# Kernel optimization log

Measured on AMD Instinct MI355X. Metric: run time of the kernel, lower is better.

Reference implementation:

```python
import jax, jax.numpy as jnp
import numpy as np

# Dims (from module defaults / forward default)
I, H, L, P = 99, 256, 2, 9   # input_size, hidden_size, num_layers, num_predictions*len(quantiles)
B, T, DEC = 64, 128, 325     # batch, encoder seq len, decoder steps (max_timesteps)


def setup_inputs() -> dict:
    key = jax.random.key(0)
    ks = jax.random.split(key, 16)
    k = 1.0 / np.sqrt(H)
    u = lambda kk, shape: jax.random.uniform(kk, shape, jnp.float32, -k, k)
    return {
        "x": jax.random.normal(ks[0], (B, T, I), jnp.float32),
        # LSTM layer 0 (input -> hidden), torch gate order i,f,g,o; b = b_ih + b_hh fused
        "W_ih0": u(ks[1], (4 * H, I)), "W_hh0": u(ks[2], (4 * H, H)), "b0": u(ks[3], (4 * H,)),
        # LSTM layer 1 (hidden -> hidden)
        "W_ih1": u(ks[4], (4 * H, H)), "W_hh1": u(ks[5], (4 * H, H)), "b1": u(ks[6], (4 * H,)),
        # linear head: ReLU -> Linear(H, I)
        "W_lin": u(ks[7], (I, H)), "b_lin": u(ks[8], (I,)),
        # prediction head: ReLU -> Linear(H, H//2) -> ReLU -> Linear(H//2, P)  (dropout = eval identity)
        "W_p1": u(ks[9], (H // 2, H)), "b_p1": u(ks[10], (H // 2,)),
        "W_p2": u(ks[11], (P, H // 2)), "b_p2": u(ks[12], (P,)),
    }


def _cell(xt, h, c, W_ih, W_hh, b):
    # single LSTM step; xt:[B,Din] h,c:[B,H]
    gates = xt @ W_ih.T + h @ W_hh.T + b
    i, f, g, o = jnp.split(gates, 4, axis=-1)
    c = jax.nn.sigmoid(f) * c + jax.nn.sigmoid(i) * jnp.tanh(g)
    h = jax.nn.sigmoid(o) * jnp.tanh(c)
    return h, c


def _lstm_seq(x, W_ih, W_hh, b, h0, c0):
    # x:[B,T,Din] -> outputs [B,T,H], final (h,c)
    xW = jnp.einsum('btd,gd->btg', x, W_ih) + b  # precompute input projection

    def step(carry, xw_t):
        h, c = carry
        gates = xw_t + h @ W_hh.T
        i, f, g, o = jnp.split(gates, 4, axis=-1)
        c = jax.nn.sigmoid(f) * c + jax.nn.sigmoid(i) * jnp.tanh(g)
        h = jax.nn.sigmoid(o) * jnp.tanh(c)
        return (h, c), h

    (h, c), hs = jax.lax.scan(step, (h0, c0), jnp.swapaxes(xW, 0, 1))
    return jnp.swapaxes(hs, 0, 1), h, c


def _lin_head(h, W, b):
    return jnp.maximum(h, 0.0) @ W.T + b


def _pred_head(h, W1, b1, W2, b2):
    z = jnp.maximum(jnp.maximum(h, 0.0) @ W1.T + b1, 0.0)
    return z @ W2.T + b2


def reference(x, W_ih0, W_hh0, b0, W_ih1, W_hh1, b1,
              W_lin, b_lin, W_p1, b_p1, W_p2, b_p2):
    Bx = x.shape[0]
    z = jnp.zeros((Bx, H), x.dtype)
    # encoder: 2-layer LSTM, zero initial state
    out0, h0_, c0_ = _lstm_seq(x, W_ih0, W_hh0, b0, z, z)
    out1, h1_, c1_ = _lstm_seq(out0, W_ih1, W_hh1, b1, z, z)

    yields_back = _pred_head(out1, W_p1, b_p1, W_p2, b_p2)        # [B,T,P]
    sensors_back = _lin_head(out1, W_lin, b_lin)                  # [B,T,I]
    dec_in = jax.lax.stop_gradient(sensors_back[:, -1, :])        # [B,I]

    def dec_step(carry, _):
        h0, c0, h1, c1, xin = carry
        h0, c0 = _cell(xin, h0, c0, W_ih0, W_hh0, b0)
        h1, c1 = _cell(h0, h1, c1, W_ih1, W_hh1, b1)
        sens = _lin_head(h1, W_lin, b_lin)                        # [B,I]
        yld = _pred_head(h1, W_p1, b_p1, W_p2, b_p2)              # [B,P]
        xin = jax.lax.stop_gradient(sens)
        return (h0, c0, h1, c1, xin), (sens, yld)

    _, (sens_fwd, yld_fwd) = jax.lax.scan(
        dec_step, (h0_, c0_, h1_, c1_, dec_in), None, length=DEC)
    sensors_forward = jnp.swapaxes(sens_fwd, 0, 1)                # [B,DEC,I]
    yields = jnp.concatenate([yields_back, jnp.swapaxes(yld_fwd, 0, 1)], axis=1)  # [B,T+DEC,P]
    return (sensors_forward, sensors_back, yields)
```

## Files before the change

kernel.cpp:

```cpp
#include <hip/hip_runtime.h>
#include <math.h>


#define NW    128
#define NTHR  256

#define II 99
#define BB 64
#define TT 128
#define DD 325
#define QTOT 453
#define PPQ 9

#define SF_OFF 0
#define SB_OFF (BB*DD*II)
#define Y_OFF  (SB_OFF + BB*TT*II)

#define WS_H0 1024
#define WS_H1 (WS_H0 + 2*256*64)
#define WS_Z  (WS_H1 + 2*256*64)
#define WS_XT (WS_Z  + 2*128*64)

#define AGENT __HIP_MEMORY_SCOPE_AGENT

__device__ __forceinline__ float sigm(float v){ return 1.0f/(1.0f+expf(-v)); }
__device__ __forceinline__ void st_wt(float* p, float v){ __hip_atomic_store(p, v, __ATOMIC_RELAXED, AGENT); }

__device__ __forceinline__ void fma32(float acc[32], float4 w0, float4 w1, float4 hv) {
  float wr[8] = {w0.x,w0.y,w0.z,w0.w,w1.x,w1.y,w1.z,w1.w};
  #pragma unroll
  for (int g = 0; g < 8; ++g) {
    acc[(g<<2)+0] += wr[g]*hv.x;
    acc[(g<<2)+1] += wr[g]*hv.y;
    acc[(g<<2)+2] += wr[g]*hv.z;
    acc[(g<<2)+3] += wr[g]*hv.w;
  }
}

__global__ __launch_bounds__(NTHR, 1)
void qcm_kernel(const float* __restrict__ x,
                const float* __restrict__ Wih0, const float* __restrict__ Whh0, const float* __restrict__ b0,
                const float* __restrict__ Wih1, const float* __restrict__ Whh1, const float* __restrict__ b1,
                const float* __restrict__ Wlin, const float* __restrict__ blin,
                const float* __restrict__ Wp1,  const float* __restrict__ bp1,
                const float* __restrict__ Wp2,  const float* __restrict__ bp2,
                float* __restrict__ out, float* __restrict__ ws)
{
  __shared__ float sWih0[II*8];
  __shared__ float sWhh0[2048];
  __shared__ float sWc  [2048];
  __shared__ float sWih1[2048];
  __shared__ float sWhh1[2048];
  __shared__ float sWlin[256];
  __shared__ float sWp1 [256];
  __shared__ float sWp2 [10*128];
  __shared__ float sGred[4*512];
  __shared__ float sGates[512];
  __shared__ float sHs[4*64];
  __shared__ float sHz[4*64];
  __shared__ float sYred[2][8];
  __shared__ float sB[48];

  int*   flags = (int*)ws;
  float* H0 = ws + WS_H0;
  float* H1 = ws + WS_H1;
  float* Zb = ws + WS_Z;
  float* XT = ws + WS_XT;

  const int wg  = (int)blockIdx.x;
  const int tid = (int)threadIdx.x;
  const int wv  = tid >> 6;
  const int ln  = tid & 63;
  const int rg  = ln >> 2;
  const int rb  = rg << 2;
  const int ks  = (wv << 2) | (ln & 3);
  const int u0  = wg << 1;

  float c0 = 0.f, c1 = 0.f;

  for (int idx = tid; idx < II*8; idx += NTHR) {
    int k = idx >> 3, g = idx & 7;
    int gate = ((g >> 1) << 8) + u0 + (g & 1);
    sWih0[idx] = Wih0[gate*II + k];
  }
  for (int idx = tid; idx < 2048; idx += NTHR) {
    int k = idx >> 3, g = idx & 7;
    int gate = ((g >> 1) << 8) + u0 + (g & 1);
    sWhh0[idx] = Whh0[(gate << 8) + k];
    sWih1[idx] = Wih1[(gate << 8) + k];
    sWhh1[idx] = Whh1[(gate << 8) + k];
  }
  sWlin[tid] = (wg < II) ? Wlin[wg*256 + tid] : 0.f;
  sWp1[tid]  = Wp1[wg*256 + tid];
  for (int idx = tid; idx < 1280; idx += NTHR) sWp2[idx] = (idx < 1152) ? Wp2[idx] : 0.f;
  if (tid < 8) {
    int gate = ((tid >> 1) << 8) + u0 + (tid & 1);
    sB[tid]      = b0[gate];
    sB[16 + tid] = b1[gate];
  }
  if (tid == 0) {
    sB[24] = (wg < II) ? blin[wg] : 0.f;
    sB[25] = bp1[wg];
  }
  if (tid < 9) sB[32 + tid] = bp2[tid];
  __syncthreads();
  for (int idx = tid; idx < 2048; idx += NTHR) {
    int k = idx >> 3, g = idx & 7;
    float a = 0.f;
    for (int j = 0; j < II; ++j) a += sWih0[(j << 3) + g] * Wlin[(j << 8) + k];
    sWc[idx] = a;
  }
  if (tid < 8) {
    float a = 0.f;
    for (int j = 0; j < II; ++j) a += sWih0[(j << 3) + tid] * blin[j];
    sB[8 + tid] = sB[tid] + a;
  }
  for (int idx = tid; idx < II*BB; idx += NTHR) {
    int b = idx & 63, i = idx >> 6;
    st_wt(&XT[(size_t)wg*(II*BB) + (i << 6) + b], x[((size_t)b*TT + wg)*II + i]);
  }
  if (tid < 128) {
    int uu = tid >> 6, r = tid & 63;
    st_wt(&H0[(size_t)((256 + u0 + uu) << 6) + r], 0.f);
    st_wt(&H1[(size_t)((256 + u0 + uu) << 6) + r], 0.f);
  }
  asm volatile("s_waitcnt vmcnt(0)" ::: "memory");
  __syncthreads();
  if (tid == 0) __hip_atomic_store(&flags[wg], 1, __ATOMIC_RELAXED, AGENT);

  int phi = 1;
  for (int ctr = 0; ctr <= 454; ++ctr) {
    ++phi;
    {
      const int tgt = phi - 1;
      if (tid < NW)
        while (__hip_atomic_load(&flags[tid], __ATOMIC_RELAXED, AGENT) < tgt)
          __builtin_amdgcn_s_sleep(2);
      __syncthreads();
      __builtin_amdgcn_fence(__ATOMIC_ACQUIRE, "agent");
    }
    const int bq = wg >> 1, pb = (wg & 1) ? 5 : 0;
    float zv = 0.f;
    if (ctr >= 2 && tid < 128)
      zv = Zb[((size_t)(ctr & 1) << 13) + ((size_t)tid << 6) + bq];

    if (ctr <= 452) {
      float acc[32];
      #pragma unroll
      for (int q2 = 0; q2 < 32; ++q2) acc[q2] = 0.f;
      const int pp = (ctr - 1) & 1;

      if (ctr < TT) {
        const float* xb = XT + (size_t)ctr * (II*BB);
        for (int k = ks; k < II; k += 16) {
          float4 hv = *(const float4*)(xb + (k << 6) + rb);
          fma32(acc, *(const float4*)(sWih0 + (k<<3)), *(const float4*)(sWih0 + (k<<3) + 4), hv);
        }
        const float* hb0 = H0 + ((size_t)pp << 14);
        #pragma unroll
        for (int m = 0; m < 16; ++m) {
          int k = ks + (m << 4);
          float4 hv = *(const float4*)(hb0 + (k << 6) + rb);
          fma32(acc, *(const float4*)(sWhh0 + (k<<3)), *(const float4*)(sWhh0 + (k<<3) + 4), hv);
        }
      } else {
        const float* hb1 = H1 + ((size_t)pp << 14);
        const float* hb0 = H0 + ((size_t)pp << 14);
        #pragma unroll
        for (int m = 0; m < 16; ++m) {
          int k = ks + (m << 4);
          float4 h1v = *(const float4*)(hb1 + (k << 6) + rb);
          float4 h0v = *(const float4*)(hb0 + (k << 6) + rb);
          h1v.x = fmaxf(h1v.x, 0.f); h1v.y = fmaxf(h1v.y, 0.f);
          h1v.z = fmaxf(h1v.z, 0.f); h1v.w = fmaxf(h1v.w, 0.f);
          fma32(acc, *(const float4*)(sWc   + (k<<3)), *(const float4*)(sWc   + (k<<3) + 4), h1v);
          fma32(acc, *(const float4*)(sWhh0 + (k<<3)), *(const float4*)(sWhh0 + (k<<3) + 4), h0v);
        }
      }
      #pragma unroll
      for (int q2 = 0; q2 < 32; ++q2) {
        float v = acc[q2];
        v += __shfl_xor(v, 1, 64); v += __shfl_xor(v, 2, 64);
        acc[q2] = v;
      }
      if ((ln & 3) == 0) {
        #pragma unroll
        for (int g = 0; g < 8; ++g)
          *(float4*)(sGred + (wv << 9) + (g << 6) + rb) =
            make_float4(acc[(g<<2)], acc[(g<<2)+1], acc[(g<<2)+2], acc[(g<<2)+3]);
      }
      if (ctr >= 2 && tid < 128) {
        float yp[5];
        #pragma unroll
        for (int p = 0; p < 5; ++p) yp[p] = zv * sWp2[((pb + p) << 7) + tid];
        #pragma unroll
        for (int p = 0; p < 5; ++p) {
          float v = yp[p];
          v += __shfl_xor(v,1,64); v += __shfl_xor(v,2,64); v += __shfl_xor(v,4,64);
          v += __shfl_xor(v,8,64); v += __shfl_xor(v,16,64); v += __shfl_xor(v,32,64);
          yp[p] = v;
        }
        if (ln == 0) {
          #pragma unroll
          for (int p = 0; p < 5; ++p) sYred[wv][p] = yp[p];
        }
      }
      __syncthreads();
      if (tid < 128) {
        const int boff = (ctr < TT) ? 0 : 8;
        float4 a0 = *(const float4*)(sGred +    0 + (tid<<2));
        float4 a1 = *(const float4*)(sGred +  512 + (tid<<2));
        float4 a2 = *(const float4*)(sGred + 1024 + (tid<<2));
        float4 a3 = *(const float4*)(sGred + 1536 + (tid<<2));
        float bias = sB[boff + (tid >> 4)];
        float4 r;
        r.x = a0.x+a1.x+a2.x+a3.x + bias;
        r.y = a0.y+a1.y+a2.y+a3.y + bias;
        r.z = a0.z+a1.z+a2.z+a3.z + bias;
        r.w = a0.w+a1.w+a2.w+a3.w + bias;
        *(float4*)(sGates + (tid<<2)) = r;
      }
      __syncthreads();
      if (tid < 128) {
        int uu = tid >> 6, r = tid & 63;
        float i_ = sigm (sGates[( uu      << 6) + r]);
        float f_ = sigm (sGates[((2 + uu) << 6) + r]);
        float g_ = tanhf(sGates[((4 + uu) << 6) + r]);
        float o_ = sigm (sGates[((6 + uu) << 6) + r]);
        float c = f_*c0 + i_*g_;
        c0 = c;
        st_wt(&H0[((size_t)(((ctr & 1) << 8) + u0 + uu) << 6) + r], o_*tanhf(c));
      }
      if (ctr >= 2 && tid >= 192 && tid < 197) {
        int p = tid - 192;
        if (pb + p < 9) {
          float y = sYred[0][p] + sYred[1][p] + sB[32 + pb + p];
          st_wt(&out[Y_OFF + ((size_t)bq*QTOT + (ctr - 2))*PPQ + pb + p], y);
        }
      }
    } else {
      if (tid < 128) {
        float yp[5];
        #pragma unroll
        for (int p = 0; p < 5; ++p) yp[p] = zv * sWp2[((pb + p) << 7) + tid];
        #pragma unroll
        for (int p = 0; p < 5; ++p) {
          float v = yp[p];
          v += __shfl_xor(v,1,64); v += __shfl_xor(v,2,64); v += __shfl_xor(v,4,64);
          v += __shfl_xor(v,8,64); v += __shfl_xor(v,16,64); v += __shfl_xor(v,32,64);
          yp[p] = v;
        }
        if (ln == 0) {
          #pragma unroll
          for (int p = 0; p < 5; ++p) sYred[wv][p] = yp[p];
        }
      }
      __syncthreads();
      if (tid >= 192 && tid < 197) {
        int p = tid - 192;
        if (pb + p < 9) {
          float y = sYred[0][p] + sYred[1][p] + sB[32 + pb + p];
          st_wt(&out[Y_OFF + ((size_t)bq*QTOT + (ctr - 2))*PPQ + pb + p], y);
        }
      }
    }
    asm volatile("s_waitcnt vmcnt(0)" ::: "memory");
    __syncthreads();
    if (tid == 0) __hip_atomic_store(&flags[wg], phi, __ATOMIC_RELAXED, AGENT);
    if (ctr == 454) break;

    ++phi;
    {
      const int tgt = phi - 1;
      if (tid < NW)
        while (__hip_atomic_load(&flags[tid], __ATOMIC_RELAXED, AGENT) < tgt)
          __builtin_amdgcn_s_sleep(2);
      __syncthreads();
      __builtin_amdgcn_fence(__ATOMIC_ACQUIRE, "agent");
    }
    {
      const int pp = (ctr - 1) & 1, cur = ctr & 1;
      float ps[4] = {0,0,0,0}, pz[4] = {0,0,0,0};

      if (ctr <= 452) {
        float acc[32];
        #pragma unroll
        for (int q2 = 0; q2 < 32; ++q2) acc[q2] = 0.f;

        const float* hbA = H0 + ((size_t)cur << 14);
        const float* hbB = H1 + ((size_t)pp  << 14);
        #pragma unroll
        for (int m = 0; m < 16; ++m) {
          int k = ks + (m << 4);
          float4 hv0 = *(const float4*)(hbA + (k << 6) + rb);
          float4 hv1 = *(const float4*)(hbB + (k << 6) + rb);
          fma32(acc, *(const float4*)(sWih1 + (k<<3)), *(const float4*)(sWih1 + (k<<3) + 4), hv0);
          fma32(acc, *(const float4*)(sWhh1 + (k<<3)), *(const float4*)(sWhh1 + (k<<3) + 4), hv1);
          float rx = fmaxf(hv1.x,0.f), ry = fmaxf(hv1.y,0.f), rz = fmaxf(hv1.z,0.f), rw = fmaxf(hv1.w,0.f);
          float wl = sWlin[k], wp = sWp1[k];
          ps[0] += rx*wl; ps[1] += ry*wl; ps[2] += rz*wl; ps[3] += rw*wl;
          pz[0] += rx*wp; pz[1] += ry*wp; pz[2] += rz*wp; pz[3] += rw*wp;
        }
        #pragma unroll
        for (int q2 = 0; q2 < 32; ++q2) {
          float v = acc[q2];
          v += __shfl_xor(v, 1, 64); v += __shfl_xor(v, 2, 64);
          acc[q2] = v;
        }
        #pragma unroll
        for (int j = 0; j < 4; ++j) {
          float v = ps[j]; v += __shfl_xor(v,1,64); v += __shfl_xor(v,2,64); ps[j] = v;
          v = pz[j]; v += __shfl_xor(v,1,64); v += __shfl_xor(v,2,64); pz[j] = v;
        }
        if ((ln & 3) == 0) {
          #pragma unroll
          for (int g = 0; g < 8; ++g)
            *(float4*)(sGred + (wv << 9) + (g << 6) + rb) =
              make_float4(acc[(g<<2)], acc[(g<<2)+1], acc[(g<<2)+2], acc[(g<<2)+3]);
          *(float4*)(sHs + (wv << 6) + rb) = make_float4(ps[0],ps[1],ps[2],ps[3]);
          *(float4*)(sHz + (wv << 6) + rb) = make_float4(pz[0],pz[1],pz[2],pz[3]);
        }
        __syncthreads();
        if (tid < 128) {
          float4 a0 = *(const float4*)(sGred +    0 + (tid<<2));
          float4 a1 = *(const float4*)(sGred +  512 + (tid<<2));
          float4 a2 = *(const float4*)(sGred + 1024 + (tid<<2));
          float4 a3 = *(const float4*)(sGred + 1536 + (tid<<2));
          float bias = sB[16 + (tid >> 4)];
          float4 r;
          r.x = a0.x+a1.x+a2.x+a3.x + bias;
          r.y = a0.y+a1.y+a2.y+a3.y + bias;
          r.z = a0.z+a1.z+a2.z+a3.z + bias;
          r.w = a0.w+a1.w+a2.w+a3.w + bias;
          *(float4*)(sGates + (tid<<2)) = r;
        } else if (tid < 192 && ctr >= 1) {
          int b = tid - 128, q = ctr - 1;
          float s = sHs[b] + sHs[64+b] + sHs[128+b] + sHs[192+b] + sB[24];
          float z = fmaxf(sHz[b] + sHz[64+b] + sHz[128+b] + sHz[192+b] + sB[25], 0.f);
          if (wg < II) {
            size_t o = (q < TT) ? (SB_OFF + ((size_t)b*TT + q)*II + wg)
                                : (SF_OFF + ((size_t)b*DD + (q - TT))*II + wg);
            st_wt(&out[o], s);
          }
          st_wt(&Zb[((size_t)(q & 1) << 13) + ((size_t)wg << 6) + b], z);
        }
        __syncthreads();
        if (tid < 128) {
          int uu = tid >> 6, r = tid & 63;
          float i_ = sigm (sGates[( uu      << 6) + r]);
          float f_ = sigm (sGates[((2 + uu) << 6) + r]);
          float g_ = tanhf(sGates[((4 + uu) << 6) + r]);
          float o_ = sigm (sGates[((6 + uu) << 6) + r]);
          float c = f_*c1 + i_*g_;
          c1 = c;
          st_wt(&H1[((size_t)((cur << 8) + u0 + uu) << 6) + r], o_*tanhf(c));
        }
      } else {
        const float* hbB = H1 + ((size_t)pp << 14);
        #pragma unroll
        for (int m = 0; m < 16; ++m) {
          int k = ks + (m << 4);
          float4 hv1 = *(const float4*)(hbB + (k << 6) + rb);
          float rx = fmaxf(hv1.x,0.f), ry = fmaxf(hv1.y,0.f), rz = fmaxf(hv1.z,0.f), rw = fmaxf(hv1.w,0.f);
          float wl = sWlin[k], wp = sWp1[k];
          ps[0] += rx*wl; ps[1] += ry*wl; ps[2] += rz*wl; ps[3] += rw*wl;
          pz[0] += rx*wp; pz[1] += ry*wp; pz[2] += rz*wp; pz[3] += rw*wp;
        }
        #pragma unroll
        for (int j = 0; j < 4; ++j) {
          float v = ps[j]; v += __shfl_xor(v,1,64); v += __shfl_xor(v,2,64); ps[j] = v;
          v = pz[j]; v += __shfl_xor(v,1,64); v += __shfl_xor(v,2,64); pz[j] = v;
        }
        if ((ln & 3) == 0) {
          *(float4*)(sHs + (wv << 6) + rb) = make_float4(ps[0],ps[1],ps[2],ps[3]);
          *(float4*)(sHz + (wv << 6) + rb) = make_float4(pz[0],pz[1],pz[2],pz[3]);
        }
        __syncthreads();
        if (tid >= 128 && tid < 192) {
          int b = tid - 128, q = ctr - 1;
          float s = sHs[b] + sHs[64+b] + sHs[128+b] + sHs[192+b] + sB[24];
          float z = fmaxf(sHz[b] + sHz[64+b] + sHz[128+b] + sHz[192+b] + sB[25], 0.f);
          if (wg < II) {
            size_t o = SF_OFF + ((size_t)b*DD + (q - TT))*II + wg;
            st_wt(&out[o], s);
          }
          st_wt(&Zb[((size_t)(q & 1) << 13) + ((size_t)wg << 6) + b], z);
        }
      }
    }
    asm volatile("s_waitcnt vmcnt(0)" ::: "memory");
    __syncthreads();
    if (tid == 0) __hip_atomic_store(&flags[wg], phi, __ATOMIC_RELAXED, AGENT);
  }
}

extern "C" void kernel_launch(void* const* d_in, const int* in_sizes, int n_in,
                              void* d_out, int out_size, void* d_ws, size_t ws_size,
                              hipStream_t stream) {
  (void)in_sizes; (void)n_in; (void)out_size; (void)ws_size;
  qcm_kernel<<<dim3(NW), dim3(NTHR), 0, stream>>>(
      (const float*)d_in[0],
      (const float*)d_in[1], (const float*)d_in[2], (const float*)d_in[3],
      (const float*)d_in[4], (const float*)d_in[5], (const float*)d_in[6],
      (const float*)d_in[7], (const float*)d_in[8],
      (const float*)d_in[9], (const float*)d_in[10],
      (const float*)d_in[11], (const float*)d_in[12],
      (float*)d_out, (float*)d_ws);
}
```

Before: 11.87 ms.

## Replace grid-wide flag barriers with per-value sequence-tagged dataflow polling

Drops the per-phase global flag barrier, in which every workgroup waited on all 128 flags. Hidden-state, z and prediction values are now stored as 64-bit pairs carrying a sequence tag, in 4-deep ring buffers, and consumers poll the exact values they need until the tags match. The x transpose into workspace is also removed, and x is read directly from global memory in the encoder step. The aim is to cut barrier latency and let workgroups run ahead independently, at the cost of doubled buffer traffic, strided uncoalesced x loads, and reliance on 64-bit atomic stores being seen as a unit.

After: 19.48 ms. +64.1%, slower.

```diff
diff --git a/kernel.cpp b/kernel.cpp
--- a/kernel.cpp
+++ b/kernel.cpp
@@ -16,17 +16,23 @@
 #define SB_OFF (BB*DD*II)
 #define Y_OFF  (SB_OFF + BB*TT*II)
 
-#define WS_H0 1024
-#define WS_H1 (WS_H0 + 2*256*64)
-#define WS_Z  (WS_H1 + 2*256*64)
-#define WS_XT (WS_Z  + 2*128*64)
+#define WS_H0P 0
+#define WS_H1P 131072
+#define WS_ZBP 262144
 
 #define AGENT __HIP_MEMORY_SCOPE_AGENT
+
+typedef float f4 __attribute__((ext_vector_type(4)));
 
 __device__ __forceinline__ float sigm(float v){ return 1.0f/(1.0f+expf(-v)); }
 __device__ __forceinline__ void st_wt(float* p, float v){ __hip_atomic_store(p, v, __ATOMIC_RELAXED, AGENT); }
 
-__device__ __forceinline__ void fma32(float acc[32], float4 w0, float4 w1, float4 hv) {
+__device__ __forceinline__ void stp(float* p, float v, unsigned s){
+  unsigned long long u = ((unsigned long long)s << 32) | (unsigned long long)__float_as_uint(v);
+  __hip_atomic_store((unsigned long long*)p, u, __ATOMIC_RELAXED, AGENT);
+}
+
+__device__ __forceinline__ void fma32(float acc[32], f4 w0, f4 w1, f4 hv) {
   float wr[8] = {w0.x,w0.y,w0.z,w0.w,w1.x,w1.y,w1.z,w1.w};
   #pragma unroll
   for (int g = 0; g < 8; ++g) {
@@ -61,11 +67,9 @@
   __shared__ float sYred[2][8];
   __shared__ float sB[48];
 
-  int*   flags = (int*)ws;
-  float* H0 = ws + WS_H0;
-  float* H1 = ws + WS_H1;
-  float* Zb = ws + WS_Z;
-  float* XT = ws + WS_XT;
+  float* H0P = ws + WS_H0P;
+  float* H1P = ws + WS_H1P;
+  float* ZBP = ws + WS_ZBP;
 
   const int wg  = (int)blockIdx.x;
   const int tid = (int)threadIdx.x;
@@ -78,6 +82,29 @@
 
   float c0 = 0.f, c1 = 0.f;
 
+  auto poll8 = [&](const float* hb, unsigned exp, int c2, f4* hv) {
+    bool ok;
+    do {
+      ok = true;
+      #pragma unroll
+      for (int j = 0; j < 8; ++j) {
+        int k = ks + (((c2<<3) + j) << 4);
+        const float* p = hb + (((size_t)(k<<6) + rb) << 1);
+        unsigned long long a = __hip_atomic_load((const unsigned long long*)(p  ), __ATOMIC_RELAXED, AGENT);
+        unsigned long long b2= __hip_atomic_load((const unsigned long long*)(p+2), __ATOMIC_RELAXED, AGENT);
+        unsigned long long c2_=__hip_atomic_load((const unsigned long long*)(p+4), __ATOMIC_RELAXED, AGENT);
+        unsigned long long d = __hip_atomic_load((const unsigned long long*)(p+6), __ATOMIC_RELAXED, AGENT);
+        hv[j].x = __uint_as_float((unsigned)a);
+        hv[j].y = __uint_as_float((unsigned)b2);
+        hv[j].z = __uint_as_float((unsigned)c2_);
+        hv[j].w = __uint_as_float((unsigned)d);
+        ok = ok & ((unsigned)(a>>32)==exp) & ((unsigned)(b2>>32)==exp)
+                & ((unsigned)(c2_>>32)==exp) & ((unsigned)(d>>32)==exp);
+      }
+      if (!ok) __builtin_amdgcn_s_sleep(1);
+    } while (!ok);
+  };
+
   for (int idx = tid; idx < II*8; idx += NTHR) {
     int k = idx >> 3, g = idx & 7;
     int gate = ((g >> 1) << 8) + u0 + (g & 1);
@@ -115,66 +142,71 @@
     for (int j = 0; j < II; ++j) a += sWih0[(j << 3) + tid] * blin[j];
     sB[8 + tid] = sB[tid] + a;
   }
-  for (int idx = tid; idx < II*BB; idx += NTHR) {
-    int b = idx & 63, i = idx >> 6;
-    st_wt(&XT[(size_t)wg*(II*BB) + (i << 6) + b], x[((size_t)b*TT + wg)*II + i]);
-  }
   if (tid < 128) {
     int uu = tid >> 6, r = tid & 63;
-    st_wt(&H0[(size_t)((256 + u0 + uu) << 6) + r], 0.f);
-    st_wt(&H1[(size_t)((256 + u0 + uu) << 6) + r], 0.f);
-  }
-  asm volatile("s_waitcnt vmcnt(0)" ::: "memory");
+    stp(H0P + ((size_t)3 << 15) + ((((size_t)(u0+uu) << 6) + r) << 1), 0.f, 0u);
+    stp(H1P + ((size_t)3 << 15) + ((((size_t)(u0+uu) << 6) + r) << 1), 0.f, 1u);
+  }
   __syncthreads();
-  if (tid == 0) __hip_atomic_store(&flags[wg], 1, __ATOMIC_RELAXED, AGENT);
-
-  int phi = 1;
+
+  const int bq = wg >> 1, pb = (wg & 1) ? 5 : 0;
+
   for (int ctr = 0; ctr <= 454; ++ctr) {
-    ++phi;
-    {
-      const int tgt = phi - 1;
-      if (tid < NW)
-        while (__hip_atomic_load(&flags[tid], __ATOMIC_RELAXED, AGENT) < tgt)
-          __builtin_amdgcn_s_sleep(2);
-      __syncthreads();
-      __builtin_amdgcn_fence(__ATOMIC_ACQUIRE, "agent");
-    }
-    const int bq = wg >> 1, pb = (wg & 1) ? 5 : 0;
-    float zv = 0.f;
-    if (ctr >= 2 && tid < 128)
-      zv = Zb[((size_t)(ctr & 1) << 13) + ((size_t)tid << 6) + bq];
-
     if (ctr <= 452) {
       float acc[32];
       #pragma unroll
       for (int q2 = 0; q2 < 32; ++q2) acc[q2] = 0.f;
-      const int pp = (ctr - 1) & 1;
+      f4 hv[8];
 
       if (ctr < TT) {
-        const float* xb = XT + (size_t)ctr * (II*BB);
-        for (int k = ks; k < II; k += 16) {
-          float4 hv = *(const float4*)(xb + (k << 6) + rb);
-          fma32(acc, *(const float4*)(sWih0 + (k<<3)), *(const float4*)(sWih0 + (k<<3) + 4), hv);
-        }
-        const float* hb0 = H0 + ((size_t)pp << 14);
-        #pragma unroll
-        for (int m = 0; m < 16; ++m) {
+        for (int m = 0; m < 7; ++m) {
           int k = ks + (m << 4);
-          float4 hv = *(const float4*)(hb0 + (k << 6) + rb);
-          fma32(acc, *(const float4*)(sWhh0 + (k<<3)), *(const float4*)(sWhh0 + (k<<3) + 4), hv);
+          if (k < II) {
+            f4 xv;
+            xv.x = x[(size_t)(rb+0)*(TT*II) + ctr*II + k];
+            xv.y = x[(size_t)(rb+1)*(TT*II) + ctr*II + k];
+            xv.z = x[(size_t)(rb+2)*(TT*II) + ctr*II + k];
+            xv.w = x[(size_t)(rb+3)*(TT*II) + ctr*II + k];
+            fma32(acc, *(const f4*)(sWih0 + (k<<3)), *(const f4*)(sWih0 + (k<<3) + 4), xv);
+          }
+        }
+        const float* hb = H0P + ((size_t)((ctr-1)&3) << 15);
+        const unsigned e0 = (unsigned)(2*ctr);
+        for (int c2 = 0; c2 < 2; ++c2) {
+          poll8(hb, e0, c2, hv);
+          #pragma unroll
+          for (int j = 0; j < 8; ++j) {
+            int k = ks + (((c2<<3)+j) << 4);
+            fma32(acc, *(const f4*)(sWhh0 + (k<<3)), *(const f4*)(sWhh0 + (k<<3) + 4), hv[j]);
+          }
         }
       } else {
-        const float* hb1 = H1 + ((size_t)pp << 14);
-        const float* hb0 = H0 + ((size_t)pp << 14);
-        #pragma unroll
-        for (int m = 0; m < 16; ++m) {
-          int k = ks + (m << 4);
-          float4 h1v = *(const float4*)(hb1 + (k << 6) + rb);
-          float4 h0v = *(const float4*)(hb0 + (k << 6) + rb);
-          h1v.x = fmaxf(h1v.x, 0.f); h1v.y = fmaxf(h1v.y, 0.f);
-          h1v.z = fmaxf(h1v.z, 0.f); h1v.w = fmaxf(h1v.w, 0.f);
-          fma32(acc, *(const float4*)(sWc   + (k<<3)), *(const float4*)(sWc   + (k<<3) + 4), h1v);
-          fma32(acc, *(const float4*)(sWhh0 + (k<<3)), *(const float4*)(sWhh0 + (k<<3) + 4), h0v);
+        {
+          const float* hb = H0P + ((size_t)((ctr-1)&3) << 15);
+          const unsigned e0 = (unsigned)(2*ctr);
+          for (int c2 = 0; c2 < 2; ++c2) {
+            poll8(hb, e0, c2, hv);
+            #pragma unroll
+            for (int j = 0; j < 8; ++j) {
+              int k = ks + (((c2<<3)+j) << 4);
+              fma32(acc, *(const f4*)(sWhh0 + (k<<3)), *(const f4*)(sWhh0 + (k<<3) + 4), hv[j]);
+            }
+          }
+        }
+        {
+          const float* hb = H1P + ((size_t)((ctr-1)&3) << 15);
+          const unsigned e1 = (unsigned)(2*ctr+1);
+          for (int c2 = 0; c2 < 2; ++c2) {
+            poll8(hb, e1, c2, hv);
+            #pragma unroll
+            for (int j = 0; j < 8; ++j) {
+              int k = ks + (((c2<<3)+j) << 4);
+              f4 h1v = hv[j];
+              h1v.x = fmaxf(h1v.x, 0.f); h1v.y = fmaxf(h1v.y, 0.f);
+              h1v.z = fmaxf(h1v.z, 0.f); h1v.w = fmaxf(h1v.w, 0.f);
+              fma32(acc, *(const f4*)(sWc + (k<<3)), *(const f4*)(sWc + (k<<3) + 4), h1v);
+            }
+          }
         }
       }
       #pragma unroll
@@ -190,6 +222,16 @@
             make_float4(acc[(g<<2)], acc[(g<<2)+1], acc[(g<<2)+2], acc[(g<<2)+3]);
       }
       if (ctr >= 2 && tid < 128) {
+        int q = ctr - 2;
+        const unsigned ez = (unsigned)(2*q+5);
+        const float* zp = ZBP + ((size_t)(q&3) << 14) + ((((size_t)tid << 6) + bq) << 1);
+        unsigned long long u;
+        for (;;) {
+          u = __hip_atomic_load((const unsigned long long*)zp, __ATOMIC_RELAXED, AGENT);
+          if ((unsigned)(u>>32) == ez) break;
+          __builtin_amdgcn_s_sleep(1);
+        }
+        float zv = __uint_as_float((unsigned)u);
         float yp[5];
         #pragma unroll
         for (int p = 0; p < 5; ++p) yp[p] = zv * sWp2[((pb + p) << 7) + tid];
@@ -229,7 +271,8 @@
         float o_ = sigm (sGates[((6 + uu) << 6) + r]);
         float c = f_*c0 + i_*g_;
         c0 = c;
-        st_wt(&H0[((size_t)(((ctr & 1) << 8) + u0 + uu) << 6) + r], o_*tanhf(c));
+        stp(H0P + ((size_t)(ctr&3) << 15) + ((((size_t)(u0+uu) << 6) + r) << 1),
+            o_*tanhf(c), (unsigned)(2*ctr+2));
       }
       if (ctr >= 2 && tid >= 192 && tid < 197) {
         int p = tid - 192;
@@ -240,6 +283,16 @@
       }
     } else {
       if (tid < 128) {
+        int q = ctr - 2;
+        const unsigned ez = (unsigned)(2*q+5);
+        const float* zp = ZBP + ((size_t)(q&3) << 14) + ((((size_t)tid << 6) + bq) << 1);
+        unsigned long long u;
+        for (;;) {
+          u = __hip_atomic_load((const unsigned long long*)zp, __ATOMIC_RELAXED, AGENT);
+          if ((unsigned)(u>>32) == ez) break;
+          __builtin_amdgcn_s_sleep(1);
+        }
+        float zv = __uint_as_float((unsigned)u);
         float yp[5];
         #pragma unroll
         for (int p = 0; p < 5; ++p) yp[p] = zv * sWp2[((pb + p) << 7) + tid];
@@ -264,42 +317,45 @@
         }
       }
     }
-    asm volatile("s_waitcnt vmcnt(0)" ::: "memory");
-    __syncthreads();
-    if (tid == 0) __hip_atomic_store(&flags[wg], phi, __ATOMIC_RELAXED, AGENT);
     if (ctr == 454) break;
 
-    ++phi;
     {
-      const int tgt = phi - 1;
-      if (tid < NW)
-        while (__hip_atomic_load(&flags[tid], __ATOMIC_RELAXED, AGENT) < tgt)
-          __builtin_amdgcn_s_sleep(2);
-      __syncthreads();
-      __builtin_amdgcn_fence(__ATOMIC_ACQUIRE, "agent");
-    }
-    {
-      const int pp = (ctr - 1) & 1, cur = ctr & 1;
       float ps[4] = {0,0,0,0}, pz[4] = {0,0,0,0};
+      f4 hv[8];
 
       if (ctr <= 452) {
         float acc[32];
         #pragma unroll
         for (int q2 = 0; q2 < 32; ++q2) acc[q2] = 0.f;
 
-        const float* hbA = H0 + ((size_t)cur << 14);
-        const float* hbB = H1 + ((size_t)pp  << 14);
-        #pragma unroll
-        for (int m = 0; m < 16; ++m) {
-          int k = ks + (m << 4);
-          float4 hv0 = *(const float4*)(hbA + (k << 6) + rb);
-          float4 hv1 = *(const float4*)(hbB + (k << 6) + rb);
-          fma32(acc, *(const float4*)(sWih1 + (k<<3)), *(const float4*)(sWih1 + (k<<3) + 4), hv0);
-          fma32(acc, *(const float4*)(sWhh1 + (k<<3)), *(const float4*)(sWhh1 + (k<<3) + 4), hv1);
-          float rx = fmaxf(hv1.x,0.f), ry = fmaxf(hv1.y,0.f), rz = fmaxf(hv1.z,0.f), rw = fmaxf(hv1.w,0.f);
-          float wl = sWlin[k], wp = sWp1[k];
-          ps[0] += rx*wl; ps[1] += ry*wl; ps[2] += rz*wl; ps[3] += rw*wl;
-          pz[0] += rx*wp; pz[1] += ry*wp; pz[2] += rz*wp; pz[3] += rw*wp;
+        {
+          const float* hb = H1P + ((size_t)((ctr-1)&3) << 15);
+          const unsigned e1 = (unsigned)(2*ctr+1);
+          for (int c2 = 0; c2 < 2; ++c2) {
+            poll8(hb, e1, c2, hv);
+            #pragma unroll
+            for (int j = 0; j < 8; ++j) {
+              int k = ks + (((c2<<3)+j) << 4);
+              f4 h1v = hv[j];
+              fma32(acc, *(const f4*)(sWhh1 + (k<<3)), *(const f4*)(sWhh1 + (k<<3) + 4), h1v);
+              float rx = fmaxf(h1v.x,0.f), ry = fmaxf(h1v.y,0.f), rz = fmaxf(h1v.z,0.f), rw = fmaxf(h1v.w,0.f);
+              float wl = sWlin[k], wp = sWp1[k];
+              ps[0] += rx*wl; ps[1] += ry*wl; ps[2] += rz*wl; ps[3] += rw*wl;
+              pz[0] += rx*wp; pz[1] += ry*wp; pz[2] += rz*wp; pz[3] += rw*wp;
+            }
+          }
+        }
+        {
+          const float* hb = H0P + ((size_t)(ctr&3) << 15);
+          const unsigned e0 = (unsigned)(2*ctr+2);
+          for (int c2 = 0; c2 < 2; ++c2) {
+            poll8(hb, e0, c2, hv);
+            #pragma unroll
+            for (int j = 0; j < 8; ++j) {
+              int k = ks + (((c2<<3)+j) << 4);
+              fma32(acc, *(const f4*)(sWih1 + (k<<3)), *(const f4*)(sWih1 + (k<<3) + 4), hv[j]);
+            }
+          }
         }
         #pragma unroll
         for (int q2 = 0; q2 < 32; ++q2) {
@@ -342,7 +398,7 @@
                                 : (SF_OFF + ((size_t)b*DD + (q - TT))*II + wg);
             st_wt(&out[o], s);
           }
-          st_wt(&Zb[((size_t)(q & 1) << 13) + ((size_t)wg << 6) + b], z);
+          stp(ZBP + ((size_t)(q&3) << 14) + ((((size_t)wg << 6) + b) << 1), z, (unsigned)(2*q+5));
         }
         __syncthreads();
         if (tid < 128) {
@@ -353,18 +409,23 @@
           float o_ = sigm (sGates[((6 + uu) << 6) + r]);
           float c = f_*c1 + i_*g_;
           c1 = c;
-          st_wt(&H1[((size_t)((cur << 8) + u0 + uu) << 6) + r], o_*tanhf(c));
+          stp(H1P + ((size_t)(ctr&3) << 15) + ((((size_t)(u0+uu) << 6) + r) << 1),
+              o_*tanhf(c), (unsigned)(2*ctr+3));
         }
       } else {
-        const float* hbB = H1 + ((size_t)pp << 14);
-        #pragma unroll
-        for (int m = 0; m < 16; ++m) {
-          int k = ks + (m << 4);
-          float4 hv1 = *(const float4*)(hbB + (k << 6) + rb);
-          float rx = fmaxf(hv1.x,0.f), ry = fmaxf(hv1.y,0.f), rz = fmaxf(hv1.z,0.f), rw = fmaxf(hv1.w,0.f);
-          float wl = sWlin[k], wp = sWp1[k];
-          ps[0] += rx*wl; ps[1] += ry*wl; ps[2] += rz*wl; ps[3] += rw*wl;
-          pz[0] += rx*wp; pz[1] += ry*wp; pz[2] += rz*wp; pz[3] += rw*wp;
+        const float* hb = H1P + ((size_t)((ctr-1)&3) << 15);
+        const unsigned e1 = (unsigned)(2*ctr+1);
+        for (int c2 = 0; c2 < 2; ++c2) {
+          poll8(hb, e1, c2, hv);
+          #pragma unroll
+          for (int j = 0; j < 8; ++j) {
+            int k = ks + (((c2<<3)+j) << 4);
+            f4 h1v = hv[j];
+            float rx = fmaxf(h1v.x,0.f), ry = fmaxf(h1v.y,0.f), rz = fmaxf(h1v.z,0.f), rw = fmaxf(h1v.w,0.f);
+            float wl = sWlin[k], wp = sWp1[k];
+            ps[0] += rx*wl; ps[1] += ry*wl; ps[2] += rz*wl; ps[3] += rw*wl;
+            pz[0] += rx*wp; pz[1] += ry*wp; pz[2] += rz*wp; pz[3] += rw*wp;
+          }
         }
         #pragma unroll
         for (int j = 0; j < 4; ++j) {
@@ -384,13 +445,10 @@
             size_t o = SF_OFF + ((size_t)b*DD + (q - TT))*II + wg;
             st_wt(&out[o], s);
           }
-          st_wt(&Zb[((size_t)(q & 1) << 13) + ((size_t)wg << 6) + b], z);
+          stp(ZBP + ((size_t)(q&3) << 14) + ((((size_t)wg << 6) + b) << 1), z, (unsigned)(2*q+5));
         }
       }
     }
-    asm volatile("s_waitcnt vmcnt(0)" ::: "memory");
-    __syncthreads();
-    if (tid == 0) __hip_atomic_store(&flags[wg], phi, __ATOMIC_RELAXED, AGENT);
   }
 }
 
```

## Replace grid-wide flag barriers with per-element sequence-tagged dataflow loads

Applied to the files above, without the earlier changes.

Removes the global flag barrier that every workgroup polled twice per step. Each hidden-state and Z value is now stored as a 64-bit word that packs the float with a step sequence number, and readers spin on only the words they need until the tag matches. The x input projection is also read directly from the input and reduced in shared memory, replacing the transposed staging copy in workspace. This lets workgroups run ahead loosely instead of in lockstep. The costs are doubled bytes per exchanged value and many small spinning atomic loads, and correctness now relies on the sequence tagging and buffer reuse being race-free.

Result: slower. 14.24 ms (+20.0%).

```diff
diff --git a/kernel.cpp b/kernel.cpp
--- a/kernel.cpp
+++ b/kernel.cpp
@@ -16,17 +16,26 @@
 #define SB_OFF (BB*DD*II)
 #define Y_OFF  (SB_OFF + BB*TT*II)
 
-#define WS_H0 1024
-#define WS_H1 (WS_H0 + 2*256*64)
-#define WS_Z  (WS_H1 + 2*256*64)
-#define WS_XT (WS_Z  + 2*128*64)
+#define WS_H0P 0
+#define WS_H1P 65536
+#define WS_ZBP 131072
 
 #define AGENT __HIP_MEMORY_SCOPE_AGENT
+
+typedef float f4 __attribute__((ext_vector_type(4)));
+typedef unsigned long long u64;
 
 __device__ __forceinline__ float sigm(float v){ return 1.0f/(1.0f+expf(-v)); }
 __device__ __forceinline__ void st_wt(float* p, float v){ __hip_atomic_store(p, v, __ATOMIC_RELAXED, AGENT); }
-
-__device__ __forceinline__ void fma32(float acc[32], float4 w0, float4 w1, float4 hv) {
+__device__ __forceinline__ void stp(float* p, float v, unsigned s){
+  u64 u = ((u64)s << 32) | (u64)__float_as_uint(v);
+  __hip_atomic_store((u64*)p, u, __ATOMIC_RELAXED, AGENT);
+}
+__device__ __forceinline__ u64 ald(const float* p){
+  return __hip_atomic_load((const u64*)p, __ATOMIC_RELAXED, AGENT);
+}
+
+__device__ __forceinline__ void fma32(float acc[32], f4 w0, f4 w1, f4 hv) {
   float wr[8] = {w0.x,w0.y,w0.z,w0.w,w1.x,w1.y,w1.z,w1.w};
   #pragma unroll
   for (int g = 0; g < 8; ++g) {
@@ -56,16 +65,15 @@
   __shared__ float sWp2 [10*128];
   __shared__ float sGred[4*512];
   __shared__ float sGates[512];
+  __shared__ float sXred[4*512];
   __shared__ float sHs[4*64];
   __shared__ float sHz[4*64];
   __shared__ float sYred[2][8];
   __shared__ float sB[48];
 
-  int*   flags = (int*)ws;
-  float* H0 = ws + WS_H0;
-  float* H1 = ws + WS_H1;
-  float* Zb = ws + WS_Z;
-  float* XT = ws + WS_XT;
+  float* H0P = ws + WS_H0P;
+  float* H1P = ws + WS_H1P;
+  float* ZBP = ws + WS_ZBP;
 
   const int wg  = (int)blockIdx.x;
   const int tid = (int)threadIdx.x;
@@ -78,6 +86,43 @@
 
   float c0 = 0.f, c1 = 0.f;
 
+  auto pass16 = [&](const float* hb, unsigned exp, auto&& use) {
+    const float* pb_ = hb + (((size_t)ks << 7) + ((size_t)rb << 1));
+    u64 pr[16][4];
+    #pragma unroll
+    for (int j = 0; j < 16; ++j) {
+      const float* p = pb_ + ((size_t)j << 11);
+      pr[j][0]=ald(p); pr[j][1]=ald(p+2); pr[j][2]=ald(p+4); pr[j][3]=ald(p+6);
+    }
+    unsigned todo = 0;
+    #pragma unroll
+    for (int j = 0; j < 16; ++j) {
+      bool ok = ((unsigned)(pr[j][0]>>32)==exp) && ((unsigned)(pr[j][1]>>32)==exp)
+             && ((unsigned)(pr[j][2]>>32)==exp) && ((unsigned)(pr[j][3]>>32)==exp);
+      if (ok) {
+        f4 v; v.x=__uint_as_float((unsigned)pr[j][0]); v.y=__uint_as_float((unsigned)pr[j][1]);
+              v.z=__uint_as_float((unsigned)pr[j][2]); v.w=__uint_as_float((unsigned)pr[j][3]);
+        use(j, v);
+      } else todo |= 1u << j;
+    }
+    while (todo) {
+      __builtin_amdgcn_s_sleep(1);
+      #pragma unroll
+      for (int j = 0; j < 16; ++j) if ((todo >> j) & 1u) {
+        const float* p = pb_ + ((size_t)j << 11);
+        u64 a=ald(p), b2=ald(p+2), c2=ald(p+4), d2=ald(p+6);
+        bool ok = ((unsigned)(a>>32)==exp) && ((unsigned)(b2>>32)==exp)
+               && ((unsigned)(c2>>32)==exp) && ((unsigned)(d2>>32)==exp);
+        if (ok) {
+          f4 v; v.x=__uint_as_float((unsigned)a); v.y=__uint_as_float((unsigned)b2);
+                v.z=__uint_as_float((unsigned)c2); v.w=__uint_as_float((unsigned)d2);
+          use(j, v);
+          todo &= ~(1u << j);
+        }
+      }
+    }
+  };
+
   for (int idx = tid; idx < II*8; idx += NTHR) {
     int k = idx >> 3, g = idx & 7;
     int gate = ((g >> 1) << 8) + u0 + (g & 1);
@@ -115,84 +160,74 @@
     for (int j = 0; j < II; ++j) a += sWih0[(j << 3) + tid] * blin[j];
     sB[8 + tid] = sB[tid] + a;
   }
-  for (int idx = tid; idx < II*BB; idx += NTHR) {
-    int b = idx & 63, i = idx >> 6;
-    st_wt(&XT[(size_t)wg*(II*BB) + (i << 6) + b], x[((size_t)b*TT + wg)*II + i]);
-  }
   if (tid < 128) {
     int uu = tid >> 6, r = tid & 63;
-    st_wt(&H0[(size_t)((256 + u0 + uu) << 6) + r], 0.f);
-    st_wt(&H1[(size_t)((256 + u0 + uu) << 6) + r], 0.f);
-  }
-  asm volatile("s_waitcnt vmcnt(0)" ::: "memory");
+    stp(H0P + ((size_t)1 << 15) + ((((size_t)(u0+uu) << 6) + r) << 1), 0.f, 0u);
+    stp(H1P + ((size_t)1 << 15) + ((((size_t)(u0+uu) << 6) + r) << 1), 0.f, 1u);
+  }
   __syncthreads();
-  if (tid == 0) __hip_atomic_store(&flags[wg], 1, __ATOMIC_RELAXED, AGENT);
-
-  int phi = 1;
+
+  const int bq = wg >> 1, pb2 = (wg & 1) ? 5 : 0;
+
   for (int ctr = 0; ctr <= 454; ++ctr) {
-    ++phi;
     {
-      const int tgt = phi - 1;
-      if (tid < NW)
-        while (__hip_atomic_load(&flags[tid], __ATOMIC_RELAXED, AGENT) < tgt)
-          __builtin_amdgcn_s_sleep(2);
-      __syncthreads();
-      __builtin_amdgcn_fence(__ATOMIC_ACQUIRE, "agent");
-    }
-    const int bq = wg >> 1, pb = (wg & 1) ? 5 : 0;
-    float zv = 0.f;
-    if (ctr >= 2 && tid < 128)
-      zv = Zb[((size_t)(ctr & 1) << 13) + ((size_t)tid << 6) + bq];
-
-    if (ctr <= 452) {
-      float acc[32];
-      #pragma unroll
-      for (int q2 = 0; q2 < 32; ++q2) acc[q2] = 0.f;
-      const int pp = (ctr - 1) & 1;
-
-      if (ctr < TT) {
-        const float* xb = XT + (size_t)ctr * (II*BB);
-        for (int k = ks; k < II; k += 16) {
-          float4 hv = *(const float4*)(xb + (k << 6) + rb);
-          fma32(acc, *(const float4*)(sWih0 + (k<<3)), *(const float4*)(sWih0 + (k<<3) + 4), hv);
-        }
-        const float* hb0 = H0 + ((size_t)pp << 14);
-        #pragma unroll
-        for (int m = 0; m < 16; ++m) {
-          int k = ks + (m << 4);
-          float4 hv = *(const float4*)(hb0 + (k << 6) + rb);
-          fma32(acc, *(const float4*)(sWhh0 + (k<<3)), *(const float4*)(sWhh0 + (k<<3) + 4), hv);
-        }
-      } else {
-        const float* hb1 = H1 + ((size_t)pp << 14);
-        const float* hb0 = H0 + ((size_t)pp << 14);
-        #pragma unroll
-        for (int m = 0; m < 16; ++m) {
-          int k = ks + (m << 4);
-          float4 h1v = *(const float4*)(hb1 + (k << 6) + rb);
-          float4 h0v = *(const float4*)(hb0 + (k << 6) + rb);
-          h1v.x = fmaxf(h1v.x, 0.f); h1v.y = fmaxf(h1v.y, 0.f);
-          h1v.z = fmaxf(h1v.z, 0.f); h1v.w = fmaxf(h1v.w, 0.f);
-          fma32(acc, *(const float4*)(sWc   + (k<<3)), *(const float4*)(sWc   + (k<<3) + 4), h1v);
-          fma32(acc, *(const float4*)(sWhh0 + (k<<3)), *(const float4*)(sWhh0 + (k<<3) + 4), h0v);
-        }
-      }
-      #pragma unroll
-      for (int q2 = 0; q2 < 32; ++q2) {
-        float v = acc[q2];
-        v += __shfl_xor(v, 1, 64); v += __shfl_xor(v, 2, 64);
-        acc[q2] = v;
-      }
-      if ((ln & 3) == 0) {
-        #pragma unroll
-        for (int g = 0; g < 8; ++g)
-          *(float4*)(sGred + (wv << 9) + (g << 6) + rb) =
-            make_float4(acc[(g<<2)], acc[(g<<2)+1], acc[(g<<2)+2], acc[(g<<2)+3]);
-      }
+      u64 zu = 0; float* zp = nullptr; unsigned ez = 0;
       if (ctr >= 2 && tid < 128) {
+        int q = ctr - 2;
+        ez = (unsigned)(2*q + 5);
+        zp = ZBP + ((size_t)(q & 1) << 14) + ((((size_t)tid << 6) + bq) << 1);
+        zu = ald(zp);
+      }
+      if (ctr <= 452) {
+        float acc[32];
+        #pragma unroll
+        for (int q2 = 0; q2 < 32; ++q2) acc[q2] = 0.f;
+
+        if (ctr < TT) {
+          float ax[8];
+          #pragma unroll
+          for (int g = 0; g < 8; ++g) ax[g] = 0.f;
+          const int kb = wv*25, kq = (wv < 3) ? 25 : 24;
+          const float* xp = x + (size_t)ln*(TT*II) + (size_t)ctr*II + kb;
+          #pragma unroll
+          for (int i = 0; i < 25; ++i) if (i < kq) {
+            float xv = xp[i];
+            #pragma unroll
+            for (int g = 0; g < 8; ++g) ax[g] += xv * sWih0[((kb+i) << 3) + g];
+          }
+          #pragma unroll
+          for (int g = 0; g < 8; ++g) sXred[(wv << 9) + (g << 6) + ln] = ax[g];
+          pass16(H0P + ((size_t)((ctr-1)&1) << 15), (unsigned)(2*ctr),
+                 [&](int j, f4 v){ int k = ks + (j << 4);
+                   fma32(acc, *(const f4*)(sWhh0 + (k<<3)), *(const f4*)(sWhh0 + (k<<3) + 4), v); });
+        } else {
+          pass16(H0P + ((size_t)((ctr-1)&1) << 15), (unsigned)(2*ctr),
+                 [&](int j, f4 v){ int k = ks + (j << 4);
+                   fma32(acc, *(const f4*)(sWhh0 + (k<<3)), *(const f4*)(sWhh0 + (k<<3) + 4), v); });
+          pass16(H1P + ((size_t)((ctr-1)&1) << 15), (unsigned)(2*ctr+1),
+                 [&](int j, f4 v){ int k = ks + (j << 4);
+                   v.x=fmaxf(v.x,0.f); v.y=fmaxf(v.y,0.f); v.z=fmaxf(v.z,0.f); v.w=fmaxf(v.w,0.f);
+                   fma32(acc, *(const f4*)(sWc + (k<<3)), *(const f4*)(sWc + (k<<3) + 4), v); });
+        }
+        #pragma unroll
+        for (int q2 = 0; q2 < 32; ++q2) {
+          float v = acc[q2];
+          v += __shfl_xor(v, 1, 64); v += __shfl_xor(v, 2, 64);
+          acc[q2] = v;
+        }
+        if ((ln & 3) == 0) {
+          #pragma unroll
+          for (int g = 0; g < 8; ++g)
+            *(float4*)(sGred + (wv << 9) + (g << 6) + rb) =
+              make_float4(acc[(g<<2)], acc[(g<<2)+1], acc[(g<<2)+2], acc[(g<<2)+3]);
+        }
+      }
+      if (ctr >= 2 && tid < 128) {
+        while ((unsigned)(zu >> 32) != ez) { __builtin_amdgcn_s_sleep(1); zu = ald(zp); }
+        float zv = __uint_as_float((unsigned)zu);
         float yp[5];
         #pragma unroll
-        for (int p = 0; p < 5; ++p) yp[p] = zv * sWp2[((pb + p) << 7) + tid];
+        for (int p = 0; p < 5; ++p) yp[p] = zv * sWp2[((pb2 + p) << 7) + tid];
         #pragma unroll
         for (int p = 0; p < 5; ++p) {
           float v = yp[p];
@@ -206,22 +241,37 @@
         }
       }
       __syncthreads();
-      if (tid < 128) {
+      if (ctr <= 452 && tid < 128) {
         const int boff = (ctr < TT) ? 0 : 8;
+        const int g = tid >> 4, bb = (tid & 15) << 2;
         float4 a0 = *(const float4*)(sGred +    0 + (tid<<2));
         float4 a1 = *(const float4*)(sGred +  512 + (tid<<2));
         float4 a2 = *(const float4*)(sGred + 1024 + (tid<<2));
         float4 a3 = *(const float4*)(sGred + 1536 + (tid<<2));
-        float bias = sB[boff + (tid >> 4)];
+        float bias = sB[boff + g];
         float4 r;
         r.x = a0.x+a1.x+a2.x+a3.x + bias;
         r.y = a0.y+a1.y+a2.y+a3.y + bias;
         r.z = a0.z+a1.z+a2.z+a3.z + bias;
         r.w = a0.w+a1.w+a2.w+a3.w + bias;
+        if (ctr < TT) {
+          #pragma unroll
+          for (int w2 = 0; w2 < 4; ++w2) {
+            float4 xr = *(const float4*)(sXred + (w2 << 9) + (g << 6) + bb);
+            r.x += xr.x; r.y += xr.y; r.z += xr.z; r.w += xr.w;
+          }
+        }
         *(float4*)(sGates + (tid<<2)) = r;
       }
+      if (ctr >= 2 && tid >= 192 && tid < 197) {
+        int p = tid - 192;
+        if (pb2 + p < 9) {
+          float y = sYred[0][p] + sYred[1][p] + sB[32 + pb2 + p];
+          st_wt(&out[Y_OFF + ((size_t)bq*QTOT + (ctr - 2))*PPQ + pb2 + p], y);
+        }
+      }
       __syncthreads();
-      if (tid < 128) {
+      if (ctr <= 452 && tid < 128) {
         int uu = tid >> 6, r = tid & 63;
         float i_ = sigm (sGates[( uu      << 6) + r]);
         float f_ = sigm (sGates[((2 + uu) << 6) + r]);
@@ -229,78 +279,30 @@
         float o_ = sigm (sGates[((6 + uu) << 6) + r]);
         float c = f_*c0 + i_*g_;
         c0 = c;
-        st_wt(&H0[((size_t)(((ctr & 1) << 8) + u0 + uu) << 6) + r], o_*tanhf(c));
-      }
-      if (ctr >= 2 && tid >= 192 && tid < 197) {
-        int p = tid - 192;
-        if (pb + p < 9) {
-          float y = sYred[0][p] + sYred[1][p] + sB[32 + pb + p];
-          st_wt(&out[Y_OFF + ((size_t)bq*QTOT + (ctr - 2))*PPQ + pb + p], y);
-        }
-      }
-    } else {
-      if (tid < 128) {
-        float yp[5];
-        #pragma unroll
-        for (int p = 0; p < 5; ++p) yp[p] = zv * sWp2[((pb + p) << 7) + tid];
-        #pragma unroll
-        for (int p = 0; p < 5; ++p) {
-          float v = yp[p];
-          v += __shfl_xor(v,1,64); v += __shfl_xor(v,2,64); v += __shfl_xor(v,4,64);
-          v += __shfl_xor(v,8,64); v += __shfl_xor(v,16,64); v += __shfl_xor(v,32,64);
-          yp[p] = v;
-        }
-        if (ln == 0) {
-          #pragma unroll
-          for (int p = 0; p < 5; ++p) sYred[wv][p] = yp[p];
-        }
-      }
-      __syncthreads();
-      if (tid >= 192 && tid < 197) {
-        int p = tid - 192;
-        if (pb + p < 9) {
-          float y = sYred[0][p] + sYred[1][p] + sB[32 + pb + p];
-          st_wt(&out[Y_OFF + ((size_t)bq*QTOT + (ctr - 2))*PPQ + pb + p], y);
-        }
+        stp(H0P + ((size_t)(ctr&1) << 15) + ((((size_t)(u0+uu) << 6) + r) << 1),
+            o_*tanhf(c), (unsigned)(2*ctr+2));
       }
     }
-    asm volatile("s_waitcnt vmcnt(0)" ::: "memory");
-    __syncthreads();
-    if (tid == 0) __hip_atomic_store(&flags[wg], phi, __ATOMIC_RELAXED, AGENT);
     if (ctr == 454) break;
 
-    ++phi;
     {
-      const int tgt = phi - 1;
-      if (tid < NW)
-        while (__hip_atomic_load(&flags[tid], __ATOMIC_RELAXED, AGENT) < tgt)
-          __builtin_amdgcn_s_sleep(2);
-      __syncthreads();
-      __builtin_amdgcn_fence(__ATOMIC_ACQUIRE, "agent");
-    }
-    {
-      const int pp = (ctr - 1) & 1, cur = ctr & 1;
-      float ps[4] = {0,0,0,0}, pz[4] = {0,0,0,0};
-
+      float ps4[4] = {0,0,0,0}, pz4[4] = {0,0,0,0};
       if (ctr <= 452) {
         float acc[32];
         #pragma unroll
         for (int q2 = 0; q2 < 32; ++q2) acc[q2] = 0.f;
 
-        const float* hbA = H0 + ((size_t)cur << 14);
-        const float* hbB = H1 + ((size_t)pp  << 14);
-        #pragma unroll
-        for (int m = 0; m < 16; ++m) {
-          int k = ks + (m << 4);
-          float4 hv0 = *(const float4*)(hbA + (k << 6) + rb);
-          float4 hv1 = *(const float4*)(hbB + (k << 6) + rb);
-          fma32(acc, *(const float4*)(sWih1 + (k<<3)), *(const float4*)(sWih1 + (k<<3) + 4), hv0);
-          fma32(acc, *(const float4*)(sWhh1 + (k<<3)), *(const float4*)(sWhh1 + (k<<3) + 4), hv1);
-          float rx = fmaxf(hv1.x,0.f), ry = fmaxf(hv1.y,0.f), rz = fmaxf(hv1.z,0.f), rw = fmaxf(hv1.w,0.f);
-          float wl = sWlin[k], wp = sWp1[k];
-          ps[0] += rx*wl; ps[1] += ry*wl; ps[2] += rz*wl; ps[3] += rw*wl;
-          pz[0] += rx*wp; pz[1] += ry*wp; pz[2] += rz*wp; pz[3] += rw*wp;
-        }
+        pass16(H1P + ((size_t)((ctr-1)&1) << 15), (unsigned)(2*ctr+1),
+               [&](int j, f4 v){ int k = ks + (j << 4);
+                 fma32(acc, *(const f4*)(sWhh1 + (k<<3)), *(const f4*)(sWhh1 + (k<<3) + 4), v);
+                 float rx=fmaxf(v.x,0.f), ry=fmaxf(v.y,0.f), rz=fmaxf(v.z,0.f), rw=fmaxf(v.w,0.f);
+                 float wl = sWlin[k], wp = sWp1[k];
+                 ps4[0]+=rx*wl; ps4[1]+=ry*wl; ps4[2]+=rz*wl; ps4[3]+=rw*wl;
+                 pz4[0]+=rx*wp; pz4[1]+=ry*wp; pz4[2]+=rz*wp; pz4[3]+=rw*wp; });
+        pass16(H0P + ((size_t)(ctr&1) << 15), (unsigned)(2*ctr+2),
+               [&](int j, f4 v){ int k = ks + (j << 4);
+                 fma32(acc, *(const f4*)(sWih1 + (k<<3)), *(const f4*)(sWih1 + (k<<3) + 4), v); });
+
         #pragma unroll
         for (int q2 = 0; q2 < 32; ++q2) {
           float v = acc[q2];
@@ -309,16 +311,16 @@
         }
         #pragma unroll
         for (int j = 0; j < 4; ++j) {
-          float v = ps[j]; v += __shfl_xor(v,1,64); v += __shfl_xor(v,2,64); ps[j] = v;
-          v = pz[j]; v += __shfl_xor(v,1,64); v += __shfl_xor(v,2,64); pz[j] = v;
+          float v = ps4[j]; v += __shfl_xor(v,1,64); v += __shfl_xor(v,2,64); ps4[j] = v;
+          v = pz4[j]; v += __shfl_xor(v,1,64); v += __shfl_xor(v,2,64); pz4[j] = v;
         }
         if ((ln & 3) == 0) {
           #pragma unroll
           for (int g = 0; g < 8; ++g)
             *(float4*)(sGred + (wv << 9) + (g << 6) + rb) =
               make_float4(acc[(g<<2)], acc[(g<<2)+1], acc[(g<<2)+2], acc[(g<<2)+3]);
-          *(float4*)(sHs + (wv << 6) + rb) = make_float4(ps[0],ps[1],ps[2],ps[3]);
-          *(float4*)(sHz + (wv << 6) + rb) = make_float4(pz[0],pz[1],pz[2],pz[3]);
+          *(float4*)(sHs + (wv << 6) + rb) = make_float4(ps4[0],ps4[1],ps4[2],ps4[3]);
+          *(float4*)(sHz + (wv << 6) + rb) = make_float4(pz4[0],pz4[1],pz4[2],pz4[3]);
         }
         __syncthreads();
         if (tid < 128) {
@@ -342,7 +344,7 @@
                                 : (SF_OFF + ((size_t)b*DD + (q - TT))*II + wg);
             st_wt(&out[o], s);
           }
-          st_wt(&Zb[((size_t)(q & 1) << 13) + ((size_t)wg << 6) + b], z);
+          stp(ZBP + ((size_t)(q&1) << 14) + ((((size_t)wg << 6) + b) << 1), z, (unsigned)(2*q+5));
         }
         __syncthreads();
         if (tid < 128) {
@@ -353,27 +355,24 @@
           float o_ = sigm (sGates[((6 + uu) << 6) + r]);
           float c = f_*c1 + i_*g_;
           c1 = c;
-          st_wt(&H1[((size_t)((cur << 8) + u0 + uu) << 6) + r], o_*tanhf(c));
+          stp(H1P + ((size_t)(ctr&1) << 15) + ((((size_t)(u0+uu) << 6) + r) << 1),
+              o_*tanhf(c), (unsigned)(2*ctr+3));
         }
       } else {
-        const float* hbB = H1 + ((size_t)pp << 14);
-        #pragma unroll
-        for (int m = 0; m < 16; ++m) {
-          int k = ks + (m << 4);
-          float4 hv1 = *(const float4*)(hbB + (k << 6) + rb);
-          float rx = fmaxf(hv1.x,0.f), ry = fmaxf(hv1.y,0.f), rz = fmaxf(hv1.z,0.f), rw = fmaxf(hv1.w,0.f);
-          float wl = sWlin[k], wp = sWp1[k];
-          ps[0] += rx*wl; ps[1] += ry*wl; ps[2] += rz*wl; ps[3] += rw*wl;
-          pz[0] += rx*wp; pz[1] += ry*wp; pz[2] += rz*wp; pz[3] += rw*wp;
-        }
+        pass16(H1P + ((size_t)((ctr-1)&1) << 15), (unsigned)(2*ctr+1),
+               [&](int j, f4 v){ int k = ks + (j << 4);
+                 float rx=fmaxf(v.x,0.f), ry=fmaxf(v.y,0.f), rz=fmaxf(v.z,0.f), rw=fmaxf(v.w,0.f);
+                 float wl = sWlin[k], wp = sWp1[k];
+                 ps4[0]+=rx*wl; ps4[1]+=ry*wl; ps4[2]+=rz*wl; ps4[3]+=rw*wl;
+                 pz4[0]+=rx*wp; pz4[1]+=ry*wp; pz4[2]+=rz*wp; pz4[3]+=rw*wp; });
         #pragma unroll
         for (int j = 0; j < 4; ++j) {
-          float v = ps[j]; v += __shfl_xor(v,1,64); v += __shfl_xor(v,2,64); ps[j] = v;
-          v = pz[j]; v += __shfl_xor(v,1,64); v += __shfl_xor(v,2,64); pz[j] = v;
+          float v = ps4[j]; v += __shfl_xor(v,1,64); v += __shfl_xor(v,2,64); ps4[j] = v;
+          v = pz4[j]; v += __shfl_xor(v,1,64); v += __shfl_xor(v,2,64); pz4[j] = v;
         }
         if ((ln & 3) == 0) {
-          *(float4*)(sHs + (wv << 6) + rb) = make_float4(ps[0],ps[1],ps[2],ps[3]);
-          *(float4*)(sHz + (wv << 6) + rb) = make_float4(pz[0],pz[1],pz[2],pz[3]);
+          *(float4*)(sHs + (wv << 6) + rb) = make_float4(ps4[0],ps4[1],ps4[2],ps4[3]);
+          *(float4*)(sHz + (wv << 6) + rb) = make_float4(pz4[0],pz4[1],pz4[2],pz4[3]);
         }
         __syncthreads();
         if (tid >= 128 && tid < 192) {
@@ -384,13 +383,11 @@
             size_t o = SF_OFF + ((size_t)b*DD + (q - TT))*II + wg;
             st_wt(&out[o], s);
           }
-          st_wt(&Zb[((size_t)(q & 1) << 13) + ((size_t)wg << 6) + b], z);
-        }
+          stp(ZBP + ((size_t)(q&1) << 14) + ((((size_t)wg << 6) + b) << 1), z, (unsigned)(2*q+5));
+        }
+        __syncthreads();
       }
     }
-    asm volatile("s_waitcnt vmcnt(0)" ::: "memory");
-    __syncthreads();
-    if (tid == 0) __hip_atomic_store(&flags[wg], phi, __ATOMIC_RELAXED, AGENT);
   }
 }
 
```
